# Optimization experiments

Hardware: AMD Instinct MI355X
Metric: run time of the kernel (lower is better)

The kernel has to match this reference:

```python
import jax, jax.numpy as jnp
import numpy as np
import math

B, T, C, H = 2, 2048, 1024, 16
HD = C // H  # head_dim = 64


def setup_inputs() -> dict:
    key = jax.random.key(0)
    ks = jax.random.split(key, 10)
    s = 1.0 / math.sqrt(C)
    x = jax.random.normal(ks[0], (B, T, C), jnp.float32)
    wq = jax.random.normal(ks[1], (C, C), jnp.float32) * s
    wk = jax.random.normal(ks[2], (C, C), jnp.float32) * s
    wv = jax.random.normal(ks[3], (C, C), jnp.float32) * s
    wo = jax.random.normal(ks[4], (C, C), jnp.float32) * s
    bq = jnp.zeros((C,), jnp.float32)
    bk = jnp.zeros((C,), jnp.float32)
    bv = jnp.zeros((C,), jnp.float32)
    bo = jnp.zeros((C,), jnp.float32)
    fractal_dim = jnp.ones((1,), jnp.float32)  # scalar fractal dimension input
    alpha = jnp.asarray(1.5, jnp.float32)
    fractal_alpha_scale = jnp.asarray(0.5, jnp.float32)
    energy_normalizer = jnp.asarray(1.0, jnp.float32)
    return {"x": x, "fractal_dim": fractal_dim, "wq": wq, "bq": bq, "wk": wk,
            "bk": bk, "wv": wv, "bv": bv, "wo": wo, "bo": bo, "alpha": alpha,
            "fractal_alpha_scale": fractal_alpha_scale,
            "energy_normalizer": energy_normalizer}


def reference(x, fractal_dim, wq, bq, wk, bk, wv, bv, wo, bo, alpha,
              fractal_alpha_scale, energy_normalizer):
    b, t, c = x.shape
    # input energy: L2 norm over channels, [b, t, 1]
    input_energy = jnp.linalg.norm(x, axis=-1, keepdims=True)
    adaptive_alpha = alpha + fractal_alpha_scale * (fractal_dim - 1.5)  # [1]

    q = (x @ wq + bq).reshape(b, t, H, HD)
    k = (x @ wk + bk).reshape(b, t, H, HD)
    v = (x @ wv + bv).reshape(b, t, H, HD)

    # per-head FFT along the time axis -> complex64
    q_fft = jnp.fft.fft(q, axis=1)
    k_fft = jnp.fft.fft(k, axis=1)
    v_fft = jnp.fft.fft(v, axis=1)

    freqs = jnp.fft.fftfreq(t).astype(jnp.float32)  # [t]
    phase = adaptive_alpha * jnp.arctan(jnp.log(jnp.abs(freqs) + 1e-10))  # [t]
    # unit-modulus complex spectral filter, broadcast [1, t, 1, 1]
    filt = jax.lax.complex(jnp.cos(phase), jnp.sin(phase))[None, :, None, None]

    qf = q_fft * filt
    kf = k_fft * filt
    vf = v_fft * filt

    # real part of complex matmul Q_f @ K_f^T, computed without complex GEMM:
    # Re(qf kf^T) = qr kr^T - qi ki^T
    inv_sqrt = np.float32(1.0 / math.sqrt(HD))
    logits = (jnp.einsum('bthd,bshd->bhts', qf.real, kf.real)
              - jnp.einsum('bthd,bshd->bhts', qf.imag, kf.imag)) * inv_sqrt
    attn = jax.nn.softmax(logits, axis=-1)  # [b, h, t, s]

    # attn is real, so Re(attn @ vf) = attn @ Re(vf); out_proj has real weights
    # so taking the real part before the projection is exact.
    attended = jnp.einsum('bhts,bshd->bthd', attn, vf.real)
    out = attended.reshape(b, t, c) @ wo + bo

    out_energy = jnp.linalg.norm(out, axis=-1, keepdims=True)
    energy_ratio = input_energy / (out_energy + 1e-8)
    return out * energy_ratio * energy_normalizer
```

## Files before the change

### kernel.cpp

```cpp
#include <hip/hip_runtime.h>
#include <math.h>


typedef _Float16 half8 __attribute__((ext_vector_type(8)));
typedef float f32x4 __attribute__((ext_vector_type(4)));
#define MFMA16 __builtin_amdgcn_mfma_f32_16x16x32_f16

__device__ inline unsigned pack_split(float v) {
    _Float16 h = (_Float16)v;
    float r = (v - (float)h) * 2048.0f;
    _Float16 l = (_Float16)r;
    union { _Float16 f; unsigned short u; } a, b;
    a.f = h; b.f = l;
    return (unsigned)a.u | ((unsigned)b.u << 16);
}
__device__ inline _Float16 lo16(unsigned u) {
    union { unsigned short s; _Float16 f; } x; x.s = (unsigned short)(u & 0xffffu); return x.f;
}
__device__ inline _Float16 hi16(unsigned u) {
    union { unsigned short s; _Float16 f; } x; x.s = (unsigned short)(u >> 16); return x.f;
}

__device__ inline void write_split(_Float16* dh, _Float16* dl, uint4 u0, uint4 u1) {
    uint4 lo, hi;
    lo.x = __builtin_amdgcn_perm(u0.y, u0.x, 0x05040100u);
    lo.y = __builtin_amdgcn_perm(u0.w, u0.z, 0x05040100u);
    lo.z = __builtin_amdgcn_perm(u1.y, u1.x, 0x05040100u);
    lo.w = __builtin_amdgcn_perm(u1.w, u1.z, 0x05040100u);
    hi.x = __builtin_amdgcn_perm(u0.y, u0.x, 0x07060302u);
    hi.y = __builtin_amdgcn_perm(u0.w, u0.z, 0x07060302u);
    hi.z = __builtin_amdgcn_perm(u1.y, u1.x, 0x07060302u);
    hi.w = __builtin_amdgcn_perm(u1.w, u1.z, 0x07060302u);
    *(uint4*)dh = lo;
    *(uint4*)dl = hi;
}

__global__ __launch_bounds__(256) void k_init_tables(
    float2* __restrict__ tw, float2* __restrict__ filt,
    const float* __restrict__ fd, const float* __restrict__ alpha,
    const float* __restrict__ fas)
{
    int i = blockIdx.x * 256 + threadIdx.x;
    double aa = (double)alpha[0] + (double)fas[0] * ((double)fd[0] - 1.5);
    if (i < 1024) {
        double ang = -2.0 * 3.14159265358979323846 * (double)i / 2048.0;
        double s, c;
        sincos(ang, &s, &c);
        tw[i] = make_float2((float)c, (float)s);
    }
    if (i < 2048) {
        double fr = (i < 1024) ? (double)i / 2048.0 : ((double)i - 2048.0) / 2048.0;
        double ph = aa * atan(log(fabs(fr) + 1e-10));
        double s, c;
        sincos(ph, &s, &c);
        filt[i] = make_float2((float)c, (float)s);
    }
}

__global__ __launch_bounds__(256) void k_prep_w3(
    const float* __restrict__ wq, const float* __restrict__ wk,
    const float* __restrict__ wv, unsigned* __restrict__ Wpk)
{
    __shared__ float tile[64][65];
    const int z = blockIdx.z;
    const float* W = (z == 0) ? wq : (z == 1) ? wk : wv;
    unsigned* dst = Wpk + (size_t)z * 1048576;
    const int kb = blockIdx.x * 64, cb = blockIdx.y * 64;
    const int t = threadIdx.x, r = t >> 4, c4 = (t & 15) * 4;
#pragma unroll
    for (int i = 0; i < 4; ++i) {
        int row = r + 16 * i;
        float4 v = *(const float4*)&W[(size_t)(kb + row) * 1024 + cb + c4];
        tile[row][c4 + 0] = v.x; tile[row][c4 + 1] = v.y;
        tile[row][c4 + 2] = v.z; tile[row][c4 + 3] = v.w;
    }
    __syncthreads();
#pragma unroll
    for (int i = 0; i < 4; ++i) {
        int crow = r + 16 * i;
        uint4 o;
        o.x = pack_split(tile[c4 + 0][crow]);
        o.y = pack_split(tile[c4 + 1][crow]);
        o.z = pack_split(tile[c4 + 2][crow]);
        o.w = pack_split(tile[c4 + 3][crow]);
        *(uint4*)&dst[(size_t)(cb + crow) * 1024 + kb + c4] = o;
    }
}

__global__ __launch_bounds__(256) void k_prep_w(
    const float* __restrict__ W, unsigned* __restrict__ Wpk)
{
    __shared__ float tile[64][65];
    const int kb = blockIdx.x * 64, cb = blockIdx.y * 64;
    const int t = threadIdx.x, r = t >> 4, c4 = (t & 15) * 4;
#pragma unroll
    for (int i = 0; i < 4; ++i) {
        int row = r + 16 * i;
        float4 v = *(const float4*)&W[(size_t)(kb + row) * 1024 + cb + c4];
        tile[row][c4 + 0] = v.x; tile[row][c4 + 1] = v.y;
        tile[row][c4 + 2] = v.z; tile[row][c4 + 3] = v.w;
    }
    __syncthreads();
#pragma unroll
    for (int i = 0; i < 4; ++i) {
        int crow = r + 16 * i;
        uint4 o;
        o.x = pack_split(tile[c4 + 0][crow]);
        o.y = pack_split(tile[c4 + 1][crow]);
        o.z = pack_split(tile[c4 + 2][crow]);
        o.w = pack_split(tile[c4 + 3][crow]);
        *(uint4*)&Wpk[(size_t)(cb + crow) * 1024 + kb + c4] = o;
    }
}

__global__ __launch_bounds__(256) void k_prep_x(
    const float* __restrict__ x, unsigned* __restrict__ xpk)
{
    const int base = blockIdx.x * 4096 + threadIdx.x * 4;
#pragma unroll
    for (int i = 0; i < 4; ++i) {
        int idx = base + i * 1024;
        float4 v = *(const float4*)&x[idx];
        uint4 o;
        o.x = pack_split(v.x); o.y = pack_split(v.y);
        o.z = pack_split(v.z); o.w = pack_split(v.w);
        *(uint4*)&xpk[idx] = o;
    }
}

__global__ __launch_bounds__(256) void k_gemm_qkv(
    const unsigned* __restrict__ xpk, const unsigned* __restrict__ wpk,
    const float* __restrict__ bq, const float* __restrict__ bk,
    const float* __restrict__ bv,
    float* __restrict__ qT, float* __restrict__ kT, float* __restrict__ vT)
{
    __shared__ __align__(16) _Float16 Ab[8][2][64][8];
    __shared__ __align__(16) _Float16 Bb[8][2][64][8];
    const int tid = threadIdx.x;
    const int mat = blockIdx.z;
    const unsigned* Apk = wpk + (size_t)mat * 1048576;
    const float* bias = (mat == 0) ? bq : (mat == 1) ? bk : bv;
    float* outp       = (mat == 0) ? qT : (mat == 1) ? kT : vT;
    const int m0 = blockIdx.x * 128, n0 = blockIdx.y * 128;
    const int w = tid >> 6, lane = tid & 63, quad = lane >> 4, l15 = lane & 15;
    const int wm = (w & 1) * 4, wn = (w >> 1) * 4;

    const int chA = tid & 3, rA = tid >> 2;
    const int flA = (rA & 15) + 16 * chA, mtA = rA >> 4;
    const unsigned* gA0 = &Apk[(size_t)(m0 + rA) * 1024 + chA * 8];
    const unsigned* gA1 = gA0 + (size_t)64 * 1024;
    const unsigned* gB0 = &xpk[(size_t)(n0 + rA) * 1024 + chA * 8];
    const unsigned* gB1 = gB0 + (size_t)64 * 1024;

    uint4 pa0 = *(const uint4*)gA0, pa1 = *(const uint4*)(gA0 + 4);
    uint4 pa2 = *(const uint4*)gA1, pa3 = *(const uint4*)(gA1 + 4);
    uint4 pb0 = *(const uint4*)gB0, pb1 = *(const uint4*)(gB0 + 4);
    uint4 pb2 = *(const uint4*)gB1, pb3 = *(const uint4*)(gB1 + 4);

    f32x4 acc1[4][4], acc2[4][4];
    const f32x4 z4 = {0.f, 0.f, 0.f, 0.f};
#pragma unroll
    for (int i = 0; i < 4; ++i)
#pragma unroll
        for (int j = 0; j < 4; ++j) { acc1[i][j] = z4; acc2[i][j] = z4; }

    for (int k0 = 0; k0 < 1024; k0 += 32) {
        __syncthreads();
        write_split(&Ab[mtA][0][flA][0],     &Ab[mtA][1][flA][0],     pa0, pa1);
        write_split(&Ab[mtA + 4][0][flA][0], &Ab[mtA + 4][1][flA][0], pa2, pa3);
        write_split(&Bb[mtA][0][flA][0],     &Bb[mtA][1][flA][0],     pb0, pb1);
        write_split(&Bb[mtA + 4][0][flA][0], &Bb[mtA + 4][1][flA][0], pb2, pb3);
        __syncthreads();
        if (k0 < 992) {
            int kn = k0 + 32;
            pa0 = *(const uint4*)(gA0 + kn); pa1 = *(const uint4*)(gA0 + kn + 4);
            pa2 = *(const uint4*)(gA1 + kn); pa3 = *(const uint4*)(gA1 + kn + 4);
            pb0 = *(const uint4*)(gB0 + kn); pb1 = *(const uint4*)(gB0 + kn + 4);
            pb2 = *(const uint4*)(gB1 + kn); pb3 = *(const uint4*)(gB1 + kn + 4);
        }
        half8 ah[4], al[4];
#pragma unroll
        for (int mt = 0; mt < 4; ++mt) {
            ah[mt] = *(half8*)&Ab[wm + mt][0][lane][0];
            al[mt] = *(half8*)&Ab[wm + mt][1][lane][0];
        }
#pragma unroll
        for (int nt = 0; nt < 4; ++nt) {
            half8 bh = *(half8*)&Bb[wn + nt][0][lane][0];
            half8 bl = *(half8*)&Bb[wn + nt][1][lane][0];
#pragma unroll
            for (int mt = 0; mt < 4; ++mt) {
                acc1[mt][nt] = MFMA16(ah[mt], bh, acc1[mt][nt], 0, 0, 0);
                acc2[mt][nt] = MFMA16(ah[mt], bl, acc2[mt][nt], 0, 0, 0);
                acc2[mt][nt] = MFMA16(al[mt], bh, acc2[mt][nt], 0, 0, 0);
            }
        }
    }
    const int b_ = n0 >> 11, t0 = n0 & 2047;
#pragma unroll
    for (int mt = 0; mt < 4; ++mt) {
#pragma unroll
        for (int r_ = 0; r_ < 4; ++r_) {
            int m = m0 + (wm + mt) * 16 + quad * 4 + r_;
            float bs = bias[m];
            float* orow = &outp[(size_t)(b_ * 1024 + m) * 2048 + t0];
#pragma unroll
            for (int nt = 0; nt < 4; ++nt) {
                float val = acc1[mt][nt][r_] + acc2[mt][nt][r_] * (1.f / 2048.f) + bs;
                orow[(wn + nt) * 16 + l15] = val;
            }
        }
    }
}

__global__ __launch_bounds__(256) void k_fft_filter(
    float* __restrict__ qT, float* __restrict__ kT, float* __restrict__ vT,
    float* __restrict__ qiT, float* __restrict__ kiT,
    const float2* __restrict__ tw, const float2* __restrict__ filt)
{
    __shared__ float2 sf[2048];
    const int bid = blockIdx.x;
    const int mat = bid >> 10;
    const int pair = bid & 1023;
    const int seq0 = pair * 2, seq1 = seq0 + 1;
    float* base = (mat == 0) ? qT : (mat == 1) ? kT : vT;
    float* src0 = base + (size_t)seq0 * 2048;
    float* src1 = base + (size_t)seq1 * 2048;
    const int tid = threadIdx.x;

    for (int i = tid; i < 2048; i += 256) {
        int j = (int)(__brev((unsigned)i) >> 21);
        sf[j] = make_float2(src0[i], src1[i]);
    }
    __syncthreads();
    for (int st = 1; st <= 11; ++st) {
        const int half = 1 << (st - 1);
        const int shift = 11 - st;
        for (int u = tid; u < 1024; u += 256) {
            int pos = u & (half - 1);
            int bi = 2 * u - pos;
            float2 w = tw[pos << shift];
            float2 a = sf[bi], b = sf[bi + half];
            float tr = w.x * b.x - w.y * b.y;
            float ti = w.x * b.y + w.y * b.x;
            sf[bi]        = make_float2(a.x + tr, a.y + ti);
            sf[bi + half] = make_float2(a.x - tr, a.y - ti);
        }
        __syncthreads();
    }
    unsigned* dr0 = (unsigned*)src0;
    unsigned* dr1 = (unsigned*)src1;
    unsigned* di0 = (mat == 0) ? (unsigned*)(qiT + (size_t)seq0 * 2048)
                               : (unsigned*)(kiT + (size_t)seq0 * 2048);
    unsigned* di1 = (mat == 0) ? (unsigned*)(qiT + (size_t)seq1 * 2048)
                               : (unsigned*)(kiT + (size_t)seq1 * 2048);
    for (int i = tid; i < 2048; i += 256) {
        float2 z  = sf[i];
        float2 zm = sf[(2048 - i) & 2047];
        float Are = 0.5f * (z.x + zm.x), Aim = 0.5f * (z.y - zm.y);
        float Bre = 0.5f * (z.y + zm.y), Bim = 0.5f * (zm.x - z.x);
        float2 f = filt[i];
        float re0 = Are * f.x - Aim * f.y, im0 = Are * f.y + Aim * f.x;
        float re1 = Bre * f.x - Bim * f.y, im1 = Bre * f.y + Bim * f.x;
        if (mat == 0) {
            dr0[i] = pack_split(0.125f * re0); di0[i] = pack_split(0.125f * im0);
            dr1[i] = pack_split(0.125f * re1); di1[i] = pack_split(0.125f * im1);
        } else if (mat == 1) {
            dr0[i] = pack_split(re0); di0[i] = pack_split(-im0);
            dr1[i] = pack_split(re1); di1[i] = pack_split(-im1);
        } else {
            dr0[i] = pack_split(re0);
            dr1[i] = pack_split(re1);
        }
    }
}

__global__ __launch_bounds__(512, 2) void k_flash(
    const unsigned* __restrict__ qpk, const unsigned* __restrict__ qipk,
    const unsigned* __restrict__ kpk, const unsigned* __restrict__ kipk,
    const unsigned* __restrict__ vpk, unsigned* __restrict__ attpk)
{
    __shared__ __align__(16) _Float16 Kbuf[2][4][4][2][64][8];
    __shared__ __align__(16) _Float16 Vbuf[2][2][4][2][64][8];

    const int tid = threadIdx.x;
    const int w = tid >> 6, lane = tid & 63;
    const int quad = lane >> 4, l15 = lane & 15;
    const int p = blockIdx.x;
    const int bh = (p & 7) * 4 + (p >> 6);
    const int tb = (p >> 3) & 7;
    const size_t bc = (size_t)bh * 64;
    const int tw0 = tb * 256 + w * 16;

    half8 aqh[2][4], aql[2][4];
#pragma unroll
    for (int rg = 0; rg < 2; ++rg) {
#pragma unroll
        for (int kc = 0; kc < 4; ++kc) {
#pragma unroll
            for (int j = 0; j < 8; ++j) {
                int d = kc * 32 + quad * 8 + j;
                int t = tw0 + rg * 128 + l15;
                unsigned u = (d < 64) ? qpk[(bc + d) * 2048 + t]
                                      : qipk[(bc + d - 64) * 2048 + t];
                aqh[rg][kc][j] = lo16(u);
                aql[rg][kc][j] = hi16(u);
            }
        }
    }

    f32x4 O1[2][4], O2[2][4];
    const f32x4 zero4 = {0.f, 0.f, 0.f, 0.f};
#pragma unroll
    for (int rg = 0; rg < 2; ++rg)
#pragma unroll
        for (int nt = 0; nt < 4; ++nt) { O1[rg][nt] = zero4; O2[rg][nt] = zero4; }
    float m_[2] = {-3e38f, -3e38f};
    float l_[2] = {0.f, 0.f};

    const int sK = tid & 63;
    const int dc0 = tid >> 6;
    const int stK = sK >> 4;
    const int kcK0 = dc0 >> 2;
    const int laneK = (sK & 15) + ((dc0 & 3) << 4);
    const unsigned* kre = &kpk[(bc + dc0 * 8) * 2048 + sK];
    const unsigned* kim = &kipk[(bc + dc0 * 8) * 2048 + sK];
    const int sc2V = tid >> 8;
    const int ntV = (tid >> 6) & 3, laneV = tid & 63;
    const int dV = ntV * 16 + (laneV & 15);
    const int s0V = sc2V * 32 + (laneV >> 4) * 4;
    const unsigned* vbase = &vpk[(bc + dV) * 2048 + s0V];

    unsigned ka0, ka1, ka2, ka3, ka4, ka5, ka6, ka7;
    unsigned kb0, kb1, kb2, kb3, kb4, kb5, kb6, kb7;
    uint4 va0, va1;
    ka0 = kre[0 * 2048]; ka1 = kre[1 * 2048];
    ka2 = kre[2 * 2048]; ka3 = kre[3 * 2048];
    ka4 = kre[4 * 2048]; ka5 = kre[5 * 2048];
    ka6 = kre[6 * 2048]; ka7 = kre[7 * 2048];
    kb0 = kim[0 * 2048]; kb1 = kim[1 * 2048];
    kb2 = kim[2 * 2048]; kb3 = kim[3 * 2048];
    kb4 = kim[4 * 2048]; kb5 = kim[5 * 2048];
    kb6 = kim[6 * 2048]; kb7 = kim[7 * 2048];
    va0 = *(const uint4*)vbase;
    va1 = *(const uint4*)(vbase + 16);
    write_split(&Kbuf[0][stK][kcK0][0][laneK][0], &Kbuf[0][stK][kcK0][1][laneK][0],
                make_uint4(ka0, ka1, ka2, ka3), make_uint4(ka4, ka5, ka6, ka7));
    write_split(&Kbuf[0][stK][kcK0 + 2][0][laneK][0], &Kbuf[0][stK][kcK0 + 2][1][laneK][0],
                make_uint4(kb0, kb1, kb2, kb3), make_uint4(kb4, kb5, kb6, kb7));
    write_split(&Vbuf[0][sc2V][ntV][0][laneV][0], &Vbuf[0][sc2V][ntV][1][laneV][0],
                va0, va1);
    kre += 64; kim += 64; vbase += 64;
    ka0 = kre[0 * 2048]; ka1 = kre[1 * 2048];
    ka2 = kre[2 * 2048]; ka3 = kre[3 * 2048];
    ka4 = kre[4 * 2048]; ka5 = kre[5 * 2048];
    ka6 = kre[6 * 2048]; ka7 = kre[7 * 2048];
    kb0 = kim[0 * 2048]; kb1 = kim[1 * 2048];
    kb2 = kim[2 * 2048]; kb3 = kim[3 * 2048];
    kb4 = kim[4 * 2048]; kb5 = kim[5 * 2048];
    kb6 = kim[6 * 2048]; kb7 = kim[7 * 2048];
    va0 = *(const uint4*)vbase;
    va1 = *(const uint4*)(vbase + 16);
    __syncthreads();

    for (int it = 0; it < 32; ++it) {
        const int cur = it & 1, nxt = cur ^ 1;
        if (it < 31) {
            write_split(&Kbuf[nxt][stK][kcK0][0][laneK][0],
                        &Kbuf[nxt][stK][kcK0][1][laneK][0],
                        make_uint4(ka0, ka1, ka2, ka3), make_uint4(ka4, ka5, ka6, ka7));
            write_split(&Kbuf[nxt][stK][kcK0 + 2][0][laneK][0],
                        &Kbuf[nxt][stK][kcK0 + 2][1][laneK][0],
                        make_uint4(kb0, kb1, kb2, kb3), make_uint4(kb4, kb5, kb6, kb7));
            write_split(&Vbuf[nxt][sc2V][ntV][0][laneV][0],
                        &Vbuf[nxt][sc2V][ntV][1][laneV][0], va0, va1);
        }
        if (it < 30) {
            kre += 64; kim += 64; vbase += 64;
            ka0 = kre[0 * 2048]; ka1 = kre[1 * 2048];
            ka2 = kre[2 * 2048]; ka3 = kre[3 * 2048];
            ka4 = kre[4 * 2048]; ka5 = kre[5 * 2048];
            ka6 = kre[6 * 2048]; ka7 = kre[7 * 2048];
            kb0 = kim[0 * 2048]; kb1 = kim[1 * 2048];
            kb2 = kim[2 * 2048]; kb3 = kim[3 * 2048];
            kb4 = kim[4 * 2048]; kb5 = kim[5 * 2048];
            kb6 = kim[6 * 2048]; kb7 = kim[7 * 2048];
            va0 = *(const uint4*)vbase;
            va1 = *(const uint4*)(vbase + 16);
        }

        f32x4 S1[2][4], S2[2][4];
#pragma unroll
        for (int rg = 0; rg < 2; ++rg)
#pragma unroll
            for (int st = 0; st < 4; ++st) { S1[rg][st] = zero4; S2[rg][st] = zero4; }
        __builtin_amdgcn_s_setprio(1);
#pragma unroll
        for (int st = 0; st < 4; ++st) {
#pragma unroll
            for (int kc = 0; kc < 4; ++kc) {
                half8 khf = *(half8*)&Kbuf[cur][st][kc][0][lane][0];
                half8 klf = *(half8*)&Kbuf[cur][st][kc][1][lane][0];
#pragma unroll
                for (int rg = 0; rg < 2; ++rg) {
                    S1[rg][st] = MFMA16(khf, aqh[rg][kc], S1[rg][st], 0, 0, 0);
                    S2[rg][st] = MFMA16(klf, aqh[rg][kc], S2[rg][st], 0, 0, 0);
                    S2[rg][st] = MFMA16(khf, aql[rg][kc], S2[rg][st], 0, 0, 0);
                }
            }
        }
        __builtin_amdgcn_s_setprio(0);

        half8 pb[2][2];
#pragma unroll
        for (int rg = 0; rg < 2; ++rg) {
#pragma unroll
            for (int st = 0; st < 4; ++st)
                S1[rg][st] = S1[rg][st] + S2[rg][st] * (1.f / 2048.f);
            float mt = -3e38f;
#pragma unroll
            for (int st = 0; st < 4; ++st)
#pragma unroll
                for (int r = 0; r < 4; ++r)
                    mt = fmaxf(mt, S1[rg][st][r]);
            mt = fmaxf(mt, __shfl_xor(mt, 16));
            mt = fmaxf(mt, __shfl_xor(mt, 32));
            if (!__all(mt <= m_[rg] + 8.f)) {
                float mn2 = fmaxf(m_[rg], mt);
                float al = __expf(m_[rg] - mn2);
                m_[rg] = mn2;
                l_[rg] *= al;
#pragma unroll
                for (int nt = 0; nt < 4; ++nt) { O1[rg][nt] *= al; O2[rg][nt] *= al; }
            }
            float mn = m_[rg];
            float rs = 0.f;
            _Float16 ph[4][4];
#pragma unroll
            for (int st = 0; st < 4; ++st)
#pragma unroll
                for (int r = 0; r < 4; ++r) {
                    float pe = __expf(S1[rg][st][r] - mn);
                    rs += pe;
                    ph[st][r] = (_Float16)pe;
                }
            rs += __shfl_xor(rs, 16);
            rs += __shfl_xor(rs, 32);
            l_[rg] += rs;
#pragma unroll
            for (int sc2 = 0; sc2 < 2; ++sc2) {
                half8 t8;
                t8[0] = ph[2 * sc2][0];     t8[1] = ph[2 * sc2][1];
                t8[2] = ph[2 * sc2][2];     t8[3] = ph[2 * sc2][3];
                t8[4] = ph[2 * sc2 + 1][0]; t8[5] = ph[2 * sc2 + 1][1];
                t8[6] = ph[2 * sc2 + 1][2]; t8[7] = ph[2 * sc2 + 1][3];
                pb[rg][sc2] = t8;
            }
        }

        __builtin_amdgcn_s_setprio(1);
#pragma unroll
        for (int sc2 = 0; sc2 < 2; ++sc2) {
#pragma unroll
            for (int nt = 0; nt < 4; ++nt) {
                half8 vh = *(half8*)&Vbuf[cur][sc2][nt][0][lane][0];
                half8 vl = *(half8*)&Vbuf[cur][sc2][nt][1][lane][0];
                O1[0][nt] = MFMA16(vh, pb[0][sc2], O1[0][nt], 0, 0, 0);
                O2[0][nt] = MFMA16(vl, pb[0][sc2], O2[0][nt], 0, 0, 0);
                O1[1][nt] = MFMA16(vh, pb[1][sc2], O1[1][nt], 0, 0, 0);
                O2[1][nt] = MFMA16(vl, pb[1][sc2], O2[1][nt], 0, 0, 0);
            }
        }
        __builtin_amdgcn_s_setprio(0);

        __syncthreads();
    }

    const int b = bh >> 4, h = bh & 15;
#pragma unroll
    for (int rg = 0; rg < 2; ++rg) {
        float inv = 1.0f / l_[rg];
        int t = tw0 + rg * 128 + l15;
        size_t row = (size_t)b * 2048 + t;
#pragma unroll
        for (int nt = 0; nt < 4; ++nt) {
#pragma unroll
            for (int r = 0; r < 4; ++r) {
                float val = (O1[rg][nt][r] + O2[rg][nt][r] * (1.f / 2048.f)) * inv;
                attpk[row * 1024 + h * 64 + nt * 16 + quad * 4 + r] = pack_split(val);
            }
        }
    }
}

__global__ __launch_bounds__(256) void k_gemm_out(
    const unsigned* __restrict__ attpk, const unsigned* __restrict__ wopk,
    const float* __restrict__ bo, float* __restrict__ out)
{
    __shared__ __align__(16) _Float16 Ab[8][2][64][8];
    __shared__ __align__(16) _Float16 Bb[8][2][64][8];
    const int tid = threadIdx.x;
    const int m0 = blockIdx.x * 128, n0 = blockIdx.y * 128;
    const int w = tid >> 6, lane = tid & 63, quad = lane >> 4, l15 = lane & 15;
    const int wm = (w & 1) * 4, wn = (w >> 1) * 4;

    const int chA = tid & 3, rA = tid >> 2;
    const int flA = (rA & 15) + 16 * chA, mtA = rA >> 4;
    const unsigned* gA0 = &attpk[(size_t)(m0 + rA) * 1024 + chA * 8];
    const unsigned* gA1 = gA0 + (size_t)64 * 1024;
    const unsigned* gB0 = &wopk[(size_t)(n0 + rA) * 1024 + chA * 8];
    const unsigned* gB1 = gB0 + (size_t)64 * 1024;

    uint4 pa0 = *(const uint4*)gA0, pa1 = *(const uint4*)(gA0 + 4);
    uint4 pa2 = *(const uint4*)gA1, pa3 = *(const uint4*)(gA1 + 4);
    uint4 pb0 = *(const uint4*)gB0, pb1 = *(const uint4*)(gB0 + 4);
    uint4 pb2 = *(const uint4*)gB1, pb3 = *(const uint4*)(gB1 + 4);

    f32x4 acc1[4][4], acc2[4][4];
    const f32x4 z4 = {0.f, 0.f, 0.f, 0.f};
#pragma unroll
    for (int i = 0; i < 4; ++i)
#pragma unroll
        for (int j = 0; j < 4; ++j) { acc1[i][j] = z4; acc2[i][j] = z4; }

    for (int k0 = 0; k0 < 1024; k0 += 32) {
        __syncthreads();
        write_split(&Ab[mtA][0][flA][0],     &Ab[mtA][1][flA][0],     pa0, pa1);
        write_split(&Ab[mtA + 4][0][flA][0], &Ab[mtA + 4][1][flA][0], pa2, pa3);
        write_split(&Bb[mtA][0][flA][0],     &Bb[mtA][1][flA][0],     pb0, pb1);
        write_split(&Bb[mtA + 4][0][flA][0], &Bb[mtA + 4][1][flA][0], pb2, pb3);
        __syncthreads();
        if (k0 < 992) {
            int kn = k0 + 32;
            pa0 = *(const uint4*)(gA0 + kn); pa1 = *(const uint4*)(gA0 + kn + 4);
            pa2 = *(const uint4*)(gA1 + kn); pa3 = *(const uint4*)(gA1 + kn + 4);
            pb0 = *(const uint4*)(gB0 + kn); pb1 = *(const uint4*)(gB0 + kn + 4);
            pb2 = *(const uint4*)(gB1 + kn); pb3 = *(const uint4*)(gB1 + kn + 4);
        }
        half8 ah[4], al[4];
#pragma unroll
        for (int mt = 0; mt < 4; ++mt) {
            ah[mt] = *(half8*)&Ab[wm + mt][0][lane][0];
            al[mt] = *(half8*)&Ab[wm + mt][1][lane][0];
        }
#pragma unroll
        for (int nt = 0; nt < 4; ++nt) {
            half8 bh = *(half8*)&Bb[wn + nt][0][lane][0];
            half8 bl = *(half8*)&Bb[wn + nt][1][lane][0];
#pragma unroll
            for (int mt = 0; mt < 4; ++mt) {
                acc1[mt][nt] = MFMA16(ah[mt], bh, acc1[mt][nt], 0, 0, 0);
                acc2[mt][nt] = MFMA16(ah[mt], bl, acc2[mt][nt], 0, 0, 0);
                acc2[mt][nt] = MFMA16(al[mt], bh, acc2[mt][nt], 0, 0, 0);
            }
        }
    }
#pragma unroll
    for (int mt = 0; mt < 4; ++mt) {
#pragma unroll
        for (int r_ = 0; r_ < 4; ++r_) {
            int m = m0 + (wm + mt) * 16 + quad * 4 + r_;
            float* orow = &out[(size_t)m * 1024 + n0];
#pragma unroll
            for (int nt = 0; nt < 4; ++nt) {
                int n = (wn + nt) * 16 + l15;
                float val = acc1[mt][nt][r_] + acc2[mt][nt][r_] * (1.f / 2048.f)
                          + bo[n0 + n];
                orow[n] = val;
            }
        }
    }
}

__global__ __launch_bounds__(256) void k_norm(
    const float* __restrict__ x, float* __restrict__ out,
    const float* __restrict__ en)
{
    const int row = blockIdx.x;
    const int tid = threadIdx.x;
    const float* xr = x + (size_t)row * 1024;
    float* orow = out + (size_t)row * 1024;
    float4 xv = *(const float4*)&xr[tid * 4];
    float4 ov = *(const float4*)&orow[tid * 4];
    float ssx = xv.x * xv.x + xv.y * xv.y + xv.z * xv.z + xv.w * xv.w;
    float sso = ov.x * ov.x + ov.y * ov.y + ov.z * ov.z + ov.w * ov.w;
#pragma unroll
    for (int m = 1; m <= 32; m <<= 1) {
        ssx += __shfl_xor(ssx, m, 64);
        sso += __shfl_xor(sso, m, 64);
    }
    __shared__ float rx[4], ro[4];
    const int wid = tid >> 6;
    if ((tid & 63) == 0) { rx[wid] = ssx; ro[wid] = sso; }
    __syncthreads();
    float tsx = rx[0] + rx[1] + rx[2] + rx[3];
    float tso = ro[0] + ro[1] + ro[2] + ro[3];
    float scale = sqrtf(tsx) / (sqrtf(tso) + 1e-8f) * en[0];
    ov.x *= scale; ov.y *= scale; ov.z *= scale; ov.w *= scale;
    *(float4*)&orow[tid * 4] = ov;
}

extern "C" void kernel_launch(void* const* d_in, const int* in_sizes, int n_in,
                              void* d_out, int out_size, void* d_ws, size_t ws_size,
                              hipStream_t stream)
{
    const float* x     = (const float*)d_in[0];
    const float* fd    = (const float*)d_in[1];
    const float* wq    = (const float*)d_in[2];
    const float* bq    = (const float*)d_in[3];
    const float* wk    = (const float*)d_in[4];
    const float* bk    = (const float*)d_in[5];
    const float* wv    = (const float*)d_in[6];
    const float* bv    = (const float*)d_in[7];
    const float* wo    = (const float*)d_in[8];
    const float* bo    = (const float*)d_in[9];
    const float* alpha = (const float*)d_in[10];
    const float* fas   = (const float*)d_in[11];
    const float* en    = (const float*)d_in[12];
    float* out = (float*)d_out;
    float* ws  = (float*)d_ws;

    float* qT  = ws;
    float* kT  = ws + (size_t)1 * 4194304;
    float* vT  = ws + (size_t)2 * 4194304;
    float* qiT = ws + (size_t)3 * 4194304;
    float* kiT = ws + (size_t)4 * 4194304;
    float* att = ws + (size_t)5 * 4194304;
    float2* tw   = (float2*)(ws + (size_t)6 * 4194304);
    float2* filt = (float2*)(ws + (size_t)6 * 4194304 + 2048);

    unsigned* wqkvpk = (unsigned*)qiT;
    unsigned* xpk    = (unsigned*)att;
    unsigned* attpk  = (unsigned*)att;
    unsigned* wopk   = (unsigned*)qT;

    k_init_tables<<<8, 256, 0, stream>>>(tw, filt, fd, alpha, fas);
    k_prep_w3<<<dim3(16, 16, 3), 256, 0, stream>>>(wq, wk, wv, wqkvpk);
    k_prep_x<<<1024, 256, 0, stream>>>(x, xpk);
    k_gemm_qkv<<<dim3(8, 32, 3), 256, 0, stream>>>(xpk, wqkvpk, bq, bk, bv,
                                                   qT, kT, vT);
    k_fft_filter<<<3072, 256, 0, stream>>>(qT, kT, vT, qiT, kiT, tw, filt);
    k_flash<<<256, 512, 0, stream>>>((const unsigned*)qT, (const unsigned*)qiT,
                                     (const unsigned*)kT, (const unsigned*)kiT,
                                     (const unsigned*)vT, attpk);
    k_prep_w<<<dim3(16, 16), 256, 0, stream>>>(wo, wopk);
    k_gemm_out<<<dim3(32, 8), 256, 0, stream>>>(attpk, wopk, bo, out);
    k_norm<<<4096, 256, 0, stream>>>(x, out, en);
}
```

Baseline: 439.2 us.

## Pre-tile split-fp16 QKV operands and load them directly into LDS

The weight and input prep kernels now write separate hi/lo fp16 planes in an MFMA-fragment-tiled layout instead of interleaved packed words. The QKV GEMM then fetches each 16x32 fragment straight into shared memory with global_load_lds, which removes the register staging and the perm-based unpacking on the LDS write path. In exchange it drops the register prefetch of the next k-tile, so global loads are no longer overlapped with MFMA work, and the x prep now goes through a shared-memory transpose.

```diff
diff --git a/kernel.cpp b/kernel.cpp
--- a/kernel.cpp
+++ b/kernel.cpp
@@ -5,6 +5,10 @@
 typedef _Float16 half8 __attribute__((ext_vector_type(8)));
 typedef float f32x4 __attribute__((ext_vector_type(4)));
 #define MFMA16 __builtin_amdgcn_mfma_f32_16x16x32_f16
+
+#define GLOAD16(g, l) __builtin_amdgcn_global_load_lds( \
+    (const __attribute__((address_space(1))) void*)(g), \
+    (__attribute__((address_space(3))) void*)(l), 16, 0, 0)
 
 __device__ inline unsigned pack_split(float v) {
     _Float16 h = (_Float16)v;
@@ -13,6 +17,10 @@
     union { _Float16 f; unsigned short u; } a, b;
     a.f = h; b.f = l;
     return (unsigned)a.u | ((unsigned)b.u << 16);
+}
+__device__ inline void split2(float v, _Float16& h, _Float16& l) {
+    h = (_Float16)v;
+    l = (_Float16)((v - (float)h) * 2048.0f);
 }
 __device__ inline _Float16 lo16(unsigned u) {
     union { unsigned short s; _Float16 f; } x; x.s = (unsigned short)(u & 0xffffu); return x.f;
@@ -57,14 +65,15 @@
     }
 }
 
-__global__ __launch_bounds__(256) void k_prep_w3(
+__global__ __launch_bounds__(256) void k_prep_wpl3(
     const float* __restrict__ wq, const float* __restrict__ wk,
-    const float* __restrict__ wv, unsigned* __restrict__ Wpk)
+    const float* __restrict__ wv, _Float16* __restrict__ wpl)
 {
     __shared__ float tile[64][65];
     const int z = blockIdx.z;
     const float* W = (z == 0) ? wq : (z == 1) ? wk : wv;
-    unsigned* dst = Wpk + (size_t)z * 1048576;
+    _Float16* Whi = wpl + (size_t)z * 2097152;
+    _Float16* Wlo = Whi + 1048576;
     const int kb = blockIdx.x * 64, cb = blockIdx.y * 64;
     const int t = threadIdx.x, r = t >> 4, c4 = (t & 15) * 4;
 #pragma unroll
@@ -76,14 +85,56 @@
     }
     __syncthreads();
 #pragma unroll
+    for (int h = 0; h < 2; ++h) {
+        int idx = t + h * 256;
+        int lane = idx & 63, kt2 = (idx >> 6) & 1, ct = idx >> 7;
+        int cl = ct * 16 + (lane & 15);
+        int kl = kt2 * 32 + ((lane >> 4) * 8);
+        half8 hv, lv;
+#pragma unroll
+        for (int j = 0; j < 8; ++j) {
+            _Float16 hh, ll;
+            split2(tile[kl + j][cl], hh, ll);
+            hv[j] = hh; lv[j] = ll;
+        }
+        size_t u = ((size_t)((cb >> 4) + ct) * 32 + (kb >> 5) + kt2) * 64 + lane;
+        *(half8*)&Whi[u * 8] = hv;
+        *(half8*)&Wlo[u * 8] = lv;
+    }
+}
+
+__global__ __launch_bounds__(256) void k_prep_xpl(
+    const float* __restrict__ x, _Float16* __restrict__ xpl)
+{
+    __shared__ float tile[64][65];
+    _Float16* Xhi = xpl;
+    _Float16* Xlo = xpl + 4194304;
+    const int nb = blockIdx.x * 64, cb = blockIdx.y * 64;
+    const int t = threadIdx.x, r = t >> 4, c4 = (t & 15) * 4;
+#pragma unroll
     for (int i = 0; i < 4; ++i) {
-        int crow = r + 16 * i;
-        uint4 o;
-        o.x = pack_split(tile[c4 + 0][crow]);
-        o.y = pack_split(tile[c4 + 1][crow]);
-        o.z = pack_split(tile[c4 + 2][crow]);
-        o.w = pack_split(tile[c4 + 3][crow]);
-        *(uint4*)&dst[(size_t)(cb + crow) * 1024 + kb + c4] = o;
+        int row = r + 16 * i;
+        float4 v = *(const float4*)&x[(size_t)(nb + row) * 1024 + cb + c4];
+        tile[row][c4 + 0] = v.x; tile[row][c4 + 1] = v.y;
+        tile[row][c4 + 2] = v.z; tile[row][c4 + 3] = v.w;
+    }
+    __syncthreads();
+#pragma unroll
+    for (int h = 0; h < 2; ++h) {
+        int idx = t + h * 256;
+        int lane = idx & 63, ct2 = (idx >> 6) & 1, ntl = (idx >> 7) & 3;
+        int nl = ntl * 16 + (lane & 15);
+        int cl = ct2 * 32 + ((lane >> 4) * 8);
+        half8 hv, lv;
+#pragma unroll
+        for (int j = 0; j < 8; ++j) {
+            _Float16 hh, ll;
+            split2(tile[nl][cl + j], hh, ll);
+            hv[j] = hh; lv[j] = ll;
+        }
+        size_t u = ((size_t)((nb >> 4) + ntl) * 32 + (cb >> 5) + ct2) * 64 + lane;
+        *(half8*)&Xhi[u * 8] = hv;
+        *(half8*)&Xlo[u * 8] = lv;
     }
 }
 
@@ -113,23 +164,8 @@
     }
 }
 
-__global__ __launch_bounds__(256) void k_prep_x(
-    const float* __restrict__ x, unsigned* __restrict__ xpk)
-{
-    const int base = blockIdx.x * 4096 + threadIdx.x * 4;
-#pragma unroll
-    for (int i = 0; i < 4; ++i) {
-        int idx = base + i * 1024;
-        float4 v = *(const float4*)&x[idx];
-        uint4 o;
-        o.x = pack_split(v.x); o.y = pack_split(v.y);
-        o.z = pack_split(v.z); o.w = pack_split(v.w);
-        *(uint4*)&xpk[idx] = o;
-    }
-}
-
 __global__ __launch_bounds__(256) void k_gemm_qkv(
-    const unsigned* __restrict__ xpk, const unsigned* __restrict__ wpk,
+    const _Float16* __restrict__ xpl, const _Float16* __restrict__ wpl,
     const float* __restrict__ bq, const float* __restrict__ bk,
     const float* __restrict__ bv,
     float* __restrict__ qT, float* __restrict__ kT, float* __restrict__ vT)
@@ -138,24 +174,22 @@
     __shared__ __align__(16) _Float16 Bb[8][2][64][8];
     const int tid = threadIdx.x;
     const int mat = blockIdx.z;
-    const unsigned* Apk = wpk + (size_t)mat * 1048576;
+    const _Float16* Ahi = wpl + (size_t)mat * 2097152;
+    const _Float16* Alo = Ahi + 1048576;
+    const _Float16* Bhi = xpl;
+    const _Float16* Blo = xpl + 4194304;
     const float* bias = (mat == 0) ? bq : (mat == 1) ? bk : bv;
     float* outp       = (mat == 0) ? qT : (mat == 1) ? kT : vT;
     const int m0 = blockIdx.x * 128, n0 = blockIdx.y * 128;
     const int w = tid >> 6, lane = tid & 63, quad = lane >> 4, l15 = lane & 15;
     const int wm = (w & 1) * 4, wn = (w >> 1) * 4;
 
-    const int chA = tid & 3, rA = tid >> 2;
-    const int flA = (rA & 15) + 16 * chA, mtA = rA >> 4;
-    const unsigned* gA0 = &Apk[(size_t)(m0 + rA) * 1024 + chA * 8];
-    const unsigned* gA1 = gA0 + (size_t)64 * 1024;
-    const unsigned* gB0 = &xpk[(size_t)(n0 + rA) * 1024 + chA * 8];
-    const unsigned* gB1 = gB0 + (size_t)64 * 1024;
-
-    uint4 pa0 = *(const uint4*)gA0, pa1 = *(const uint4*)(gA0 + 4);
-    uint4 pa2 = *(const uint4*)gA1, pa3 = *(const uint4*)(gA1 + 4);
-    uint4 pb0 = *(const uint4*)gB0, pb1 = *(const uint4*)(gB0 + 4);
-    uint4 pb2 = *(const uint4*)gB1, pb3 = *(const uint4*)(gB1 + 4);
+    const int s0 = 2 * w, s1 = 2 * w + 1;
+    const size_t aT0 = (size_t)((m0 >> 4) + s0) * 32;
+    const size_t aT1 = aT0 + 32;
+    const size_t bT0 = (size_t)((n0 >> 4) + s0) * 32;
+    const size_t bT1 = bT0 + 32;
+    const int ln8 = lane * 8;
 
     f32x4 acc1[4][4], acc2[4][4];
     const f32x4 z4 = {0.f, 0.f, 0.f, 0.f};
@@ -164,20 +198,23 @@
 #pragma unroll
         for (int j = 0; j < 4; ++j) { acc1[i][j] = z4; acc2[i][j] = z4; }
 
-    for (int k0 = 0; k0 < 1024; k0 += 32) {
+    for (int kt = 0; kt < 32; ++kt) {
         __syncthreads();
-        write_split(&Ab[mtA][0][flA][0],     &Ab[mtA][1][flA][0],     pa0, pa1);
-        write_split(&Ab[mtA + 4][0][flA][0], &Ab[mtA + 4][1][flA][0], pa2, pa3);
-        write_split(&Bb[mtA][0][flA][0],     &Bb[mtA][1][flA][0],     pb0, pb1);
-        write_split(&Bb[mtA + 4][0][flA][0], &Bb[mtA + 4][1][flA][0], pb2, pb3);
+        {
+            size_t oA0 = (aT0 + kt) * 512 + ln8;
+            size_t oA1 = (aT1 + kt) * 512 + ln8;
+            size_t oB0 = (bT0 + kt) * 512 + ln8;
+            size_t oB1 = (bT1 + kt) * 512 + ln8;
+            GLOAD16(Ahi + oA0, &Ab[s0][0][0][0]);
+            GLOAD16(Alo + oA0, &Ab[s0][1][0][0]);
+            GLOAD16(Ahi + oA1, &Ab[s1][0][0][0]);
+            GLOAD16(Alo + oA1, &Ab[s1][1][0][0]);
+            GLOAD16(Bhi + oB0, &Bb[s0][0][0][0]);
+            GLOAD16(Blo + oB0, &Bb[s0][1][0][0]);
+            GLOAD16(Bhi + oB1, &Bb[s1][0][0][0]);
+            GLOAD16(Blo + oB1, &Bb[s1][1][0][0]);
+        }
         __syncthreads();
-        if (k0 < 992) {
-            int kn = k0 + 32;
-            pa0 = *(const uint4*)(gA0 + kn); pa1 = *(const uint4*)(gA0 + kn + 4);
-            pa2 = *(const uint4*)(gA1 + kn); pa3 = *(const uint4*)(gA1 + kn + 4);
-            pb0 = *(const uint4*)(gB0 + kn); pb1 = *(const uint4*)(gB0 + kn + 4);
-            pb2 = *(const uint4*)(gB1 + kn); pb3 = *(const uint4*)(gB1 + kn + 4);
-        }
         half8 ah[4], al[4];
 #pragma unroll
         for (int mt = 0; mt < 4; ++mt) {
@@ -629,15 +666,15 @@
     float2* tw   = (float2*)(ws + (size_t)6 * 4194304);
     float2* filt = (float2*)(ws + (size_t)6 * 4194304 + 2048);
 
-    unsigned* wqkvpk = (unsigned*)qiT;
-    unsigned* xpk    = (unsigned*)att;
+    _Float16* wpl = (_Float16*)qiT;
+    _Float16* xpl = (_Float16*)att;
     unsigned* attpk  = (unsigned*)att;
     unsigned* wopk   = (unsigned*)qT;
 
     k_init_tables<<<8, 256, 0, stream>>>(tw, filt, fd, alpha, fas);
-    k_prep_w3<<<dim3(16, 16, 3), 256, 0, stream>>>(wq, wk, wv, wqkvpk);
-    k_prep_x<<<1024, 256, 0, stream>>>(x, xpk);
-    k_gemm_qkv<<<dim3(8, 32, 3), 256, 0, stream>>>(xpk, wqkvpk, bq, bk, bv,
+    k_prep_wpl3<<<dim3(16, 16, 3), 256, 0, stream>>>(wq, wk, wv, wpl);
+    k_prep_xpl<<<dim3(64, 16), 256, 0, stream>>>(x, xpl);
+    k_gemm_qkv<<<dim3(8, 32, 3), 256, 0, stream>>>(xpl, wpl, bq, bk, bv,
                                                    qT, kT, vT);
     k_fft_filter<<<3072, 256, 0, stream>>>(qT, kT, vT, qiT, kiT, tw, filt);
     k_flash<<<256, 512, 0, stream>>>((const unsigned*)qT, (const unsigned*)qiT,
```

Result: slower. 453.8 us (+3.3%).
